# Kernel optimization log

Measured on AMD Instinct MI355X. Metric: run time of the kernel, lower is better.

## Reference

```python
import jax, jax.numpy as jnp
import numpy as np

N_NODES = 100000
N_EDGES = 1600000
D_IN = 64
D_HID = 64
D_OUT = 64


def _sage_conv(x, src, dst, n_nodes, W_l, b_l, W_r):
    # mean aggregation of source features at destination nodes
    msgs = x[src]  # [E, F] gather
    agg = jax.ops.segment_sum(msgs, dst, num_segments=n_nodes)
    cnt = jax.ops.segment_sum(jnp.ones((src.shape[0],), x.dtype), dst, num_segments=n_nodes)
    mean = agg / jnp.maximum(cnt, 1.0)[:, None]  # nodes with no in-edges -> 0
    # out = lin_l(mean) + lin_r(x); lin_l has bias, lin_r does not (PyG default)
    return mean @ W_l.T + b_l + x @ W_r.T


def setup_inputs() -> dict:
    key = jax.random.key(0)
    ks = jax.random.split(key, 8)
    x = jax.random.normal(ks[0], (N_NODES, D_IN), dtype=jnp.float32)
    edge_index = jax.random.randint(ks[1], (2, N_EDGES), 0, N_NODES, dtype=jnp.int64) if jax.config.jax_enable_x64 else jax.random.randint(ks[1], (2, N_EDGES), 0, N_NODES, dtype=jnp.int32)
    s1 = 1.0 / np.sqrt(D_IN)
    s2 = 1.0 / np.sqrt(D_HID)
    W1_l = jax.random.uniform(ks[2], (D_HID, D_IN), jnp.float32, -s1, s1)
    b1_l = jax.random.uniform(ks[3], (D_HID,), jnp.float32, -s1, s1)
    W1_r = jax.random.uniform(ks[4], (D_HID, D_IN), jnp.float32, -s1, s1)
    W2_l = jax.random.uniform(ks[5], (D_OUT, D_HID), jnp.float32, -s2, s2)
    b2_l = jax.random.uniform(ks[6], (D_OUT,), jnp.float32, -s2, s2)
    W2_r = jax.random.uniform(ks[7], (D_OUT, D_HID), jnp.float32, -s2, s2)
    return {"x": x, "edge_index": edge_index, "W1_l": W1_l, "b1_l": b1_l, "W1_r": W1_r,
            "W2_l": W2_l, "b2_l": b2_l, "W2_r": W2_r}


def reference(x, edge_index, W1_l, b1_l, W1_r, W2_l, b2_l, W2_r):
    src, dst = edge_index[0], edge_index[1]
    h = _sage_conv(x, src, dst, x.shape[0], W1_l, b1_l, W1_r)
    h = jax.nn.relu(h)
    out = _sage_conv(h, src, dst, x.shape[0], W2_l, b2_l, W2_r)
    return out
```

## Files before the change

kernel.cpp:

```cpp
#include <hip/hip_runtime.h>
#include <hip/hip_fp16.h>

#define N_NODES 100000
#define N_EDGES 1600000
#define D 64

#define BSHIFT 8
#define BUCK_N 256
#define NBUCK 391
#define EPB 4096
#define NBLKA 391
#define SCAN_N (NBUCK * NBLKA)
#define SCAN_B1 ((SCAN_N + 255) / 256)
#define A4_CAP 6144
#define X_OCTETS (N_NODES * D / 8)

typedef _Float16 half8 __attribute__((ext_vector_type(8)));
typedef float floatx4 __attribute__((ext_vector_type(4)));


__device__ __forceinline__ uint4 pack8h(float4 a, float4 b) {
    __half2 h0, h1, h2, h3;
    h0.x = __float2half(a.x); h0.y = __float2half(a.y);
    h1.x = __float2half(a.z); h1.y = __float2half(a.w);
    h2.x = __float2half(b.x); h2.y = __float2half(b.y);
    h3.x = __float2half(b.z); h3.y = __float2half(b.w);
    uint4 pk;
    pk.x = *(unsigned int*)&h0; pk.y = *(unsigned int*)&h1;
    pk.z = *(unsigned int*)&h2; pk.w = *(unsigned int*)&h3;
    return pk;
}

__global__ void cvt_all_k(const float* __restrict__ x,
                          const float* __restrict__ W1l, const float* __restrict__ W1r,
                          const float* __restrict__ W2l, const float* __restrict__ W2r,
                          __half* __restrict__ x16,
                          __half* __restrict__ o1l, __half* __restrict__ o1r,
                          __half* __restrict__ o2l, __half* __restrict__ o2r) {
    int i = blockIdx.x * blockDim.x + threadIdx.x;
    const float* s;
    __half* d;
    int j;
    if (i < X_OCTETS) {
        s = x; d = x16; j = i * 8;
    } else {
        int k = i - X_OCTETS;
        if (k >= 2048) return;
        int arr = k >> 9;
        j = (k & 511) * 8;
        s = (arr == 0) ? W1l : (arr == 1) ? W1r : (arr == 2) ? W2l : W2r;
        d = (arr == 0) ? o1l : (arr == 1) ? o1r : (arr == 2) ? o2l : o2r;
    }
    float4 a = *(const float4*)&s[j];
    float4 b = *(const float4*)&s[j + 4];
    *(uint4*)&d[j] = pack8h(a, b);
}


__global__ void a1_hist_k(const int* __restrict__ dst, int* __restrict__ histG, int e) {
    __shared__ int hl[512];
    int t = threadIdx.x;
    hl[t] = 0;
    __syncthreads();
    int base = blockIdx.x * EPB;
#pragma unroll
    for (int r = 0; r < 8; r++) {
        int idx = base + r * 512 + t;
        if (idx < e) atomicAdd(&hl[dst[idx] >> BSHIFT], 1);
    }
    __syncthreads();
    if (t < NBUCK) histG[t * NBLKA + blockIdx.x] = hl[t];
}


__global__ void scan1_k(int* __restrict__ data, int* __restrict__ bsums, int n) {
    __shared__ int sm[256];
    int i = blockIdx.x * 256 + threadIdx.x;
    int v = (i < n) ? data[i] : 0;
    sm[threadIdx.x] = v;
    __syncthreads();
    for (int off = 1; off < 256; off <<= 1) {
        int t = (threadIdx.x >= off) ? sm[threadIdx.x - off] : 0;
        __syncthreads();
        sm[threadIdx.x] += t;
        __syncthreads();
    }
    if (i < n) data[i] = sm[threadIdx.x] - v;
    if (threadIdx.x == 255) bsums[blockIdx.x] = sm[255];
}

__global__ void scan2_k(int* __restrict__ bsums, int nb) {
    __shared__ int sm[1024];
    int v = (threadIdx.x < nb) ? bsums[threadIdx.x] : 0;
    sm[threadIdx.x] = v;
    __syncthreads();
    for (int off = 1; off < 1024; off <<= 1) {
        int t = (threadIdx.x >= off) ? sm[threadIdx.x - off] : 0;
        __syncthreads();
        sm[threadIdx.x] += t;
        __syncthreads();
    }
    if (threadIdx.x < nb) bsums[threadIdx.x] = sm[threadIdx.x];
}

__device__ __forceinline__ int hist_abs(const int* histG, const int* bsums, int idx) {
    int v = histG[idx];
    int blk = idx >> 8;
    if (blk > 0) v += bsums[blk - 1];
    return v;
}


__global__ void a3_sort_k(const int* __restrict__ src, const int* __restrict__ dst,
                          const int* __restrict__ histG, const int* __restrict__ bsums,
                          unsigned int* __restrict__ epacked, int e) {
    __shared__ int hl[512];
    __shared__ int cur[512];
    __shared__ int sc[512];
    __shared__ int gbase[NBUCK];
    __shared__ unsigned int spk[EPB];
    __shared__ unsigned short sb[EPB];
    int t = threadIdx.x;
    int blk = blockIdx.x;
    int base = blk * EPB;

    hl[t] = 0;
    __syncthreads();

    int myd[8], mys[8];
#pragma unroll
    for (int r = 0; r < 8; r++) {
        int idx = base + r * 512 + t;
        if (idx < e) {
            myd[r] = dst[idx];
            mys[r] = src[idx];
            atomicAdd(&hl[myd[r] >> BSHIFT], 1);
        } else {
            myd[r] = -1; mys[r] = 0;
        }
    }
    __syncthreads();

    int v = hl[t];
    sc[t] = v;
    __syncthreads();
    for (int off = 1; off < 512; off <<= 1) {
        int tt = (t >= off) ? sc[t - off] : 0;
        __syncthreads();
        sc[t] += tt;
        __syncthreads();
    }
    int excl = sc[t] - v;
    hl[t] = excl;
    cur[t] = excl;
    if (t < NBUCK) gbase[t] = hist_abs(histG, bsums, t * NBLKA + blk);
    __syncthreads();

#pragma unroll
    for (int r = 0; r < 8; r++) {
        if (myd[r] >= 0) {
            int b = myd[r] >> BSHIFT;
            int dl = myd[r] & (BUCK_N - 1);
            int pos = atomicAdd(&cur[b], 1);
            spk[pos] = ((unsigned)dl << 17) | (unsigned)mys[r];
            sb[pos] = (unsigned short)b;
        }
    }
    __syncthreads();

    int cnt = e - base; if (cnt > EPB) cnt = EPB;
#pragma unroll
    for (int r = 0; r < 8; r++) {
        int i = r * 512 + t;
        if (i < cnt) {
            int b = sb[i];
            epacked[gbase[b] + (i - hl[b])] = spk[i];
        }
    }
}


__global__ void a4_nodesort_k(unsigned int* __restrict__ epk,
                              const int* __restrict__ histG, const int* __restrict__ bsums,
                              int* __restrict__ row_ptr) {
    __shared__ int sorted[A4_CAP];
    __shared__ int hist[256];
    __shared__ int cur[256];
    __shared__ int sc[512];
    int b = blockIdx.x;
    int t = threadIdx.x;

    int s0 = hist_abs(histG, bsums, b * NBLKA);
    int s1 = (b == NBUCK - 1) ? N_EDGES : hist_abs(histG, bsums, (b + 1) * NBLKA);
    int cnt = s1 - s0;
    if (cnt > A4_CAP) cnt = A4_CAP;

    if (t < 256) hist[t] = 0;
    __syncthreads();

    unsigned int my[12];
    int mycnt = 0;
    for (int i = t; i < cnt; i += 512) {
        unsigned int p = epk[s0 + i];
        my[mycnt++] = p;
        atomicAdd(&hist[p >> 17], 1);
    }
    __syncthreads();

    int v = (t < 256) ? hist[t] : 0;
    sc[t] = v;
    __syncthreads();
    for (int off = 1; off < 512; off <<= 1) {
        int tt = (t >= off) ? sc[t - off] : 0;
        __syncthreads();
        sc[t] += tt;
        __syncthreads();
    }
    int start = sc[t] - v;
    if (t < 256) cur[t] = start;
    __syncthreads();

    for (int i = 0; i < mycnt; i++) {
        unsigned int p = my[i];
        int pos = atomicAdd(&cur[p >> 17], 1);
        sorted[pos] = (int)(p & 0x1FFFF);
    }
    __syncthreads();

    for (int i = t; i < cnt; i += 512) epk[s0 + i] = (unsigned int)sorted[i];

    if (t < 256) {
        int g = (b << BSHIFT) + t;
        if (g < N_NODES) row_ptr[g] = s0 + start;
    }
    if (b == NBUCK - 1 && t == 0) row_ptr[N_NODES] = N_EDGES;
}


__device__ __forceinline__ void addp(__half2* a, uint4 v) {
    const __half2* h = (const __half2*)&v;
    a[0] = __hadd2(a[0], h[0]);
    a[1] = __hadd2(a[1], h[1]);
    a[2] = __hadd2(a[2], h[2]);
    a[3] = __hadd2(a[3], h[3]);
}

__global__ void agg9_k(const __half* __restrict__ feat16,
                       const int* __restrict__ row_ptr,
                       const int* __restrict__ adj,
                       __half* __restrict__ mean16, int n) {
    int t = threadIdx.x;
    int lane = t & 63;
    int w = t >> 6;
    int node = blockIdx.x * 32 + w * 8 + (lane >> 3);
    if (node >= n) return;
    int fp = lane & 7;
    const uint4* f16 = (const uint4*)feat16;

    int beg = row_ptr[node];
    int end = row_ptr[node + 1];
    __half2 z; z.x = __float2half(0.f); z.y = z.x;
    __half2 aA[4] = {z, z, z, z};
    __half2 aB[4] = {z, z, z, z};

    int e = beg;
    for (; e + 7 < end; e += 8) {
        uint4 v0 = f16[(size_t)adj[e] * 8 + fp];
        uint4 v1 = f16[(size_t)adj[e + 1] * 8 + fp];
        uint4 v2 = f16[(size_t)adj[e + 2] * 8 + fp];
        uint4 v3 = f16[(size_t)adj[e + 3] * 8 + fp];
        uint4 v4 = f16[(size_t)adj[e + 4] * 8 + fp];
        uint4 v5 = f16[(size_t)adj[e + 5] * 8 + fp];
        uint4 v6 = f16[(size_t)adj[e + 6] * 8 + fp];
        uint4 v7 = f16[(size_t)adj[e + 7] * 8 + fp];
        addp(aA, v0); addp(aB, v1); addp(aA, v2); addp(aB, v3);
        addp(aA, v4); addp(aB, v5); addp(aA, v6); addp(aB, v7);
    }
    if (e + 3 < end) {
        uint4 v0 = f16[(size_t)adj[e] * 8 + fp];
        uint4 v1 = f16[(size_t)adj[e + 1] * 8 + fp];
        uint4 v2 = f16[(size_t)adj[e + 2] * 8 + fp];
        uint4 v3 = f16[(size_t)adj[e + 3] * 8 + fp];
        addp(aA, v0); addp(aB, v1); addp(aA, v2); addp(aB, v3);
        e += 4;
    }
    for (; e < end; e++) addp(aA, f16[(size_t)adj[e] * 8 + fp]);

    int dg = end - beg;
    float inv = (dg > 1) ? 1.0f / (float)dg : 1.0f;
    float2 s0 = __half22float2(aA[0]), s1 = __half22float2(aA[1]);
    float2 s2 = __half22float2(aA[2]), s3 = __half22float2(aA[3]);
    float2 t0 = __half22float2(aB[0]), t1 = __half22float2(aB[1]);
    float2 t2 = __half22float2(aB[2]), t3 = __half22float2(aB[3]);
    float4 o0, o1;
    o0.x = (s0.x + t0.x) * inv; o0.y = (s0.y + t0.y) * inv;
    o0.z = (s1.x + t1.x) * inv; o0.w = (s1.y + t1.y) * inv;
    o1.x = (s2.x + t2.x) * inv; o1.y = (s2.y + t2.y) * inv;
    o1.z = (s3.x + t3.x) * inv; o1.w = (s3.y + t3.y) * inv;
    *(uint4*)&mean16[(size_t)node * D + 8 * fp] = pack8h(o0, o1);
}


#define NT 4

__global__ void gemm_mfma_k(const __half* __restrict__ Ap,
                            const __half* __restrict__ Fp,
                            const __half* __restrict__ Wl16,
                            const __half* __restrict__ Wr16,
                            const float* __restrict__ bl,
                            float* __restrict__ out32,
                            __half* __restrict__ out16,
                            int n, int do_relu) {
    int t = threadIdx.x;
    int wave = t >> 6;
    int lane = t & 63;
    int fcol = lane & 15;
    int quad = lane >> 4;
    int f = wave * 16 + fcol;

    half8 b0 = *(const half8*)(Wl16 + (size_t)f * 64 + quad * 8);
    half8 b1 = *(const half8*)(Wl16 + (size_t)f * 64 + 32 + quad * 8);
    half8 b2 = *(const half8*)(Wr16 + (size_t)f * 64 + quad * 8);
    half8 b3 = *(const half8*)(Wr16 + (size_t)f * 64 + 32 + quad * 8);
    float bias = bl[f];

    int ntiles = (n + 15) >> 4;
#pragma unroll
    for (int i = 0; i < NT; i++) {
        int tile = blockIdx.x * NT + i;
        if (tile >= ntiles) break;
        size_t arow = (size_t)(tile * 16 + fcol) * 64 + quad * 8;
        half8 a0 = *(const half8*)(Ap + arow);
        half8 a1 = *(const half8*)(Ap + arow + 32);
        half8 a2 = *(const half8*)(Fp + arow);
        half8 a3 = *(const half8*)(Fp + arow + 32);

        floatx4 acc = {0.f, 0.f, 0.f, 0.f};
        acc = __builtin_amdgcn_mfma_f32_16x16x32_f16(a0, b0, acc, 0, 0, 0);
        acc = __builtin_amdgcn_mfma_f32_16x16x32_f16(a1, b1, acc, 0, 0, 0);
        acc = __builtin_amdgcn_mfma_f32_16x16x32_f16(a2, b2, acc, 0, 0, 0);
        acc = __builtin_amdgcn_mfma_f32_16x16x32_f16(a3, b3, acc, 0, 0, 0);

#pragma unroll
        for (int r = 0; r < 4; r++) {
            int node = tile * 16 + quad * 4 + r;
            if (node >= n) break;
            float v = acc[r] + bias;
            if (do_relu) v = fmaxf(v, 0.f);
            if (out32) out32[(size_t)node * 64 + f] = v;
            if (out16) out16[(size_t)node * 64 + f] = __float2half(v);
        }
    }
}

extern "C" void kernel_launch(void* const* d_in, const int* in_sizes, int n_in,
                              void* d_out, int out_size, void* d_ws, size_t ws_size,
                              hipStream_t stream) {
    const float* x   = (const float*)d_in[0];
    const int*   ei  = (const int*)d_in[1];
    const float* W1l = (const float*)d_in[2];
    const float* b1l = (const float*)d_in[3];
    const float* W1r = (const float*)d_in[4];
    const float* W2l = (const float*)d_in[5];
    const float* b2l = (const float*)d_in[6];
    const float* W2r = (const float*)d_in[7];
    float* out = (float*)d_out;

    const int* src = ei;
    const int* dst = ei + N_EDGES;

    __half* agg16 = (__half*)d_ws;
    __half* x16   = agg16 + (size_t)N_NODES * D;
    __half* h16   = x16 + (size_t)N_NODES * D;
    __half* w1l16 = h16 + (size_t)N_NODES * D;
    __half* w1r16 = w1l16 + 4096;
    __half* w2l16 = w1r16 + 4096;
    __half* w2r16 = w2l16 + 4096;
    int*   histG = (int*)(w2r16 + 4096);
    int*   bsums = histG + SCAN_N;
    int*   row_ptr = bsums + 1024;
    unsigned int* epk = (unsigned int*)(row_ptr + N_NODES + 2);

    int cvb = (X_OCTETS + 2048 + 255) / 256;
    cvt_all_k<<<cvb, 256, 0, stream>>>(x, W1l, W1r, W2l, W2r,
                                       x16, w1l16, w1r16, w2l16, w2r16);

    a1_hist_k<<<NBLKA, 512, 0, stream>>>(dst, histG, N_EDGES);
    scan1_k<<<SCAN_B1, 256, 0, stream>>>(histG, bsums, SCAN_N);
    scan2_k<<<1, 1024, 0, stream>>>(bsums, SCAN_B1);
    a3_sort_k<<<NBLKA, 512, 0, stream>>>(src, dst, histG, bsums, epk, N_EDGES);
    a4_nodesort_k<<<NBUCK, 512, 0, stream>>>(epk, histG, bsums, row_ptr);

    int ab = (N_NODES + 31) / 32;
    int gmb = ((N_NODES + 15) / 16 + NT - 1) / NT;

    agg9_k<<<ab, 256, 0, stream>>>(x16, row_ptr, (const int*)epk, agg16, N_NODES);
    gemm_mfma_k<<<gmb, 256, 0, stream>>>(agg16, x16, w1l16, w1r16, b1l,
                                         (float*)nullptr, h16, N_NODES, 1);
    agg9_k<<<ab, 256, 0, stream>>>(h16, row_ptr, (const int*)epk, agg16, N_NODES);
    gemm_mfma_k<<<gmb, 256, 0, stream>>>(agg16, h16, w2l16, w2r16, b2l,
                                         out, (__half*)nullptr, N_NODES, 0);
}
```

Baseline: 217.1 us.

## Fuse histogram into conversion kernel, sort adjacency by source bin, shuffle-broadcast neighbor indices

Merges the fp16 conversion and the destination histogram into one launch by assigning block ranges to each job. The per-bucket node sort now also orders each node's edges by the high bits of the source index, using 2048 sub-bins, so neighbor gathers in aggregation touch memory with more locality. In the aggregation loop each lane loads one adjacency index and the eight indices are broadcast with shuffles, replacing eight redundant per-lane loads. The costs are a larger shared-memory footprint in the node sort and a more involved scan.

```diff
diff --git a/kernel.cpp b/kernel.cpp
--- a/kernel.cpp
+++ b/kernel.cpp
@@ -14,6 +14,8 @@
 #define SCAN_B1 ((SCAN_N + 255) / 256)
 #define A4_CAP 6144
 #define X_OCTETS (N_NODES * D / 8)
+#define NBIN 2048
+#define CVT_BLKS ((X_OCTETS + 2048 + 511) / 512)
 
 typedef _Float16 half8 __attribute__((ext_vector_type(8)));
 typedef float floatx4 __attribute__((ext_vector_type(4)));
@@ -31,13 +33,30 @@
     return pk;
 }
 
-__global__ void cvt_all_k(const float* __restrict__ x,
-                          const float* __restrict__ W1l, const float* __restrict__ W1r,
-                          const float* __restrict__ W2l, const float* __restrict__ W2r,
-                          __half* __restrict__ x16,
-                          __half* __restrict__ o1l, __half* __restrict__ o1r,
-                          __half* __restrict__ o2l, __half* __restrict__ o2r) {
-    int i = blockIdx.x * blockDim.x + threadIdx.x;
+
+__global__ void pre_k(const float* __restrict__ x,
+                      const float* __restrict__ W1l, const float* __restrict__ W1r,
+                      const float* __restrict__ W2l, const float* __restrict__ W2r,
+                      const int* __restrict__ dst, int* __restrict__ histG,
+                      __half* __restrict__ x16,
+                      __half* __restrict__ o1l, __half* __restrict__ o1r,
+                      __half* __restrict__ o2l, __half* __restrict__ o2r) {
+    __shared__ int hl[512];
+    int t = threadIdx.x;
+    if (blockIdx.x < NBLKA) {
+        hl[t] = 0;
+        __syncthreads();
+        int base = blockIdx.x * EPB;
+#pragma unroll
+        for (int r = 0; r < 8; r++) {
+            int idx = base + r * 512 + t;
+            if (idx < N_EDGES) atomicAdd(&hl[dst[idx] >> BSHIFT], 1);
+        }
+        __syncthreads();
+        if (t < NBUCK) histG[t * NBLKA + blockIdx.x] = hl[t];
+        return;
+    }
+    int i = (blockIdx.x - NBLKA) * 512 + t;
     const float* s;
     __half* d;
     int j;
@@ -57,22 +76,6 @@
 }
 
 
-__global__ void a1_hist_k(const int* __restrict__ dst, int* __restrict__ histG, int e) {
-    __shared__ int hl[512];
-    int t = threadIdx.x;
-    hl[t] = 0;
-    __syncthreads();
-    int base = blockIdx.x * EPB;
-#pragma unroll
-    for (int r = 0; r < 8; r++) {
-        int idx = base + r * 512 + t;
-        if (idx < e) atomicAdd(&hl[dst[idx] >> BSHIFT], 1);
-    }
-    __syncthreads();
-    if (t < NBUCK) histG[t * NBLKA + blockIdx.x] = hl[t];
-}
-
-
 __global__ void scan1_k(int* __restrict__ data, int* __restrict__ bsums, int n) {
     __shared__ int sm[256];
     int i = blockIdx.x * 256 + threadIdx.x;
@@ -184,8 +187,8 @@
                               const int* __restrict__ histG, const int* __restrict__ bsums,
                               int* __restrict__ row_ptr) {
     __shared__ int sorted[A4_CAP];
-    __shared__ int hist[256];
-    __shared__ int cur[256];
+    __shared__ int hist[NBIN];
+    __shared__ int cur[NBIN];
     __shared__ int sc[512];
     int b = blockIdx.x;
     int t = threadIdx.x;
@@ -195,7 +198,8 @@
     int cnt = s1 - s0;
     if (cnt > A4_CAP) cnt = A4_CAP;
 
-    if (t < 256) hist[t] = 0;
+#pragma unroll
+    for (int i = 0; i < NBIN / 512; i++) hist[t + i * 512] = 0;
     __syncthreads();
 
     unsigned int my[12];
@@ -203,12 +207,14 @@
     for (int i = t; i < cnt; i += 512) {
         unsigned int p = epk[s0 + i];
         my[mycnt++] = p;
-        atomicAdd(&hist[p >> 17], 1);
-    }
-    __syncthreads();
-
-    int v = (t < 256) ? hist[t] : 0;
-    sc[t] = v;
+        atomicAdd(&hist[((p >> 17) << 3) | ((p & 0x1FFFFu) >> 14)], 1);
+    }
+    __syncthreads();
+
+    int b0 = t << 2;
+    int h0 = hist[b0], h1 = hist[b0 + 1], h2 = hist[b0 + 2], h3 = hist[b0 + 3];
+    int s = h0 + h1 + h2 + h3;
+    sc[t] = s;
     __syncthreads();
     for (int off = 1; off < 512; off <<= 1) {
         int tt = (t >= off) ? sc[t - off] : 0;
@@ -216,23 +222,28 @@
         sc[t] += tt;
         __syncthreads();
     }
-    int start = sc[t] - v;
-    if (t < 256) cur[t] = start;
+    int base = sc[t] - s;
+    cur[b0] = base;
+    cur[b0 + 1] = base + h0;
+    cur[b0 + 2] = base + h0 + h1;
+    cur[b0 + 3] = base + h0 + h1 + h2;
+    __syncthreads();
+
+    if (t < 256) {
+        int g = (b << BSHIFT) + t;
+        if (g < N_NODES) row_ptr[g] = s0 + cur[t << 3];
+    }
     __syncthreads();
 
     for (int i = 0; i < mycnt; i++) {
         unsigned int p = my[i];
-        int pos = atomicAdd(&cur[p >> 17], 1);
+        int pos = atomicAdd(&cur[((p >> 17) << 3) | ((p & 0x1FFFFu) >> 14)], 1);
         sorted[pos] = (int)(p & 0x1FFFF);
     }
     __syncthreads();
 
     for (int i = t; i < cnt; i += 512) epk[s0 + i] = (unsigned int)sorted[i];
 
-    if (t < 256) {
-        int g = (b << BSHIFT) + t;
-        if (g < N_NODES) row_ptr[g] = s0 + start;
-    }
     if (b == NBUCK - 1 && t == 0) row_ptr[N_NODES] = N_EDGES;
 }
 
@@ -255,6 +266,7 @@
     int node = blockIdx.x * 32 + w * 8 + (lane >> 3);
     if (node >= n) return;
     int fp = lane & 7;
+    int gl = lane & 56;
     const uint4* f16 = (const uint4*)feat16;
 
     int beg = row_ptr[node];
@@ -265,14 +277,23 @@
 
     int e = beg;
     for (; e + 7 < end; e += 8) {
-        uint4 v0 = f16[(size_t)adj[e] * 8 + fp];
-        uint4 v1 = f16[(size_t)adj[e + 1] * 8 + fp];
-        uint4 v2 = f16[(size_t)adj[e + 2] * 8 + fp];
-        uint4 v3 = f16[(size_t)adj[e + 3] * 8 + fp];
-        uint4 v4 = f16[(size_t)adj[e + 4] * 8 + fp];
-        uint4 v5 = f16[(size_t)adj[e + 5] * 8 + fp];
-        uint4 v6 = f16[(size_t)adj[e + 6] * 8 + fp];
-        uint4 v7 = f16[(size_t)adj[e + 7] * 8 + fp];
+        int am = adj[e + fp];
+        int n0 = __shfl(am, gl + 0);
+        int n1 = __shfl(am, gl + 1);
+        int n2 = __shfl(am, gl + 2);
+        int n3 = __shfl(am, gl + 3);
+        int n4 = __shfl(am, gl + 4);
+        int n5 = __shfl(am, gl + 5);
+        int n6 = __shfl(am, gl + 6);
+        int n7 = __shfl(am, gl + 7);
+        uint4 v0 = f16[(size_t)n0 * 8 + fp];
+        uint4 v1 = f16[(size_t)n1 * 8 + fp];
+        uint4 v2 = f16[(size_t)n2 * 8 + fp];
+        uint4 v3 = f16[(size_t)n3 * 8 + fp];
+        uint4 v4 = f16[(size_t)n4 * 8 + fp];
+        uint4 v5 = f16[(size_t)n5 * 8 + fp];
+        uint4 v6 = f16[(size_t)n6 * 8 + fp];
+        uint4 v7 = f16[(size_t)n7 * 8 + fp];
         addp(aA, v0); addp(aB, v1); addp(aA, v2); addp(aB, v3);
         addp(aA, v4); addp(aB, v5); addp(aA, v6); addp(aB, v7);
     }
@@ -381,11 +402,9 @@
     int*   row_ptr = bsums + 1024;
     unsigned int* epk = (unsigned int*)(row_ptr + N_NODES + 2);
 
-    int cvb = (X_OCTETS + 2048 + 255) / 256;
-    cvt_all_k<<<cvb, 256, 0, stream>>>(x, W1l, W1r, W2l, W2r,
-                                       x16, w1l16, w1r16, w2l16, w2r16);
-
-    a1_hist_k<<<NBLKA, 512, 0, stream>>>(dst, histG, N_EDGES);
+    pre_k<<<NBLKA + CVT_BLKS, 512, 0, stream>>>(x, W1l, W1r, W2l, W2r, dst, histG,
+                                                x16, w1l16, w1r16, w2l16, w2r16);
+
     scan1_k<<<SCAN_B1, 256, 0, stream>>>(histG, bsums, SCAN_N);
     scan2_k<<<1, 1024, 0, stream>>>(bsums, SCAN_B1);
     a3_sort_k<<<NBLKA, 512, 0, stream>>>(src, dst, histG, bsums, epk, N_EDGES);
```

Measured after the change: 214.8 us. No clear change (-1.0%).
